# Optimization experiments

Measured on AMD Instinct MI355X. Metric: run time of the kernel, lower is better.

## Reference

```python
import jax, jax.numpy as jnp
import numpy as np

B, Lq, Lkv = 4, 1024, 4096
Cq, Ckv, E, NH = 512, 512, 512, 8
HD = E // NH


def setup_inputs() -> dict:
    key = jax.random.key(0)
    ks = jax.random.split(key, 8)
    s = 0.02
    return {
        "Xq": jax.random.normal(ks[0], (B, Lq, Cq), dtype=jnp.float32),
        "Xkv": jax.random.normal(ks[1], (B, Lkv, Ckv), dtype=jnp.float32),
        "mask": jax.random.randint(ks[2], (B, Lq, 1), 0, 2, dtype=jnp.int32),
        "Wq": jax.random.normal(ks[3], (Cq, E), dtype=jnp.float32) * s,
        "bq": jnp.zeros((E,), dtype=jnp.float32),
        "Wkv": jax.random.normal(ks[4], (Ckv, 2 * E), dtype=jnp.float32) * s,
        "bkv": jnp.zeros((2 * E,), dtype=jnp.float32),
        "Wp": jax.random.normal(ks[5], (E, E), dtype=jnp.float32) * s,
        "bp": jnp.zeros((E,), dtype=jnp.float32),
        "attn_pos": jax.random.normal(ks[6], (1, NH, Lq, Lkv), dtype=jnp.float32) * s,
    }


def reference(Xq, Xkv, mask, Wq, bq, Wkv, bkv, Wp, bp, attn_pos):
    scale = HD ** -0.5
    # projections
    Q = (Xq @ Wq + bq).reshape(B, Lq, NH, HD).transpose(0, 2, 1, 3) * scale  # [B,NH,Lq,HD]
    KV = (Xkv @ Wkv + bkv).reshape(B, Lkv, 2, NH, HD)
    K = KV[:, :, 0].transpose(0, 2, 1, 3)  # [B,NH,Lkv,HD]
    V = KV[:, :, 1].transpose(0, 2, 1, 3)
    # scores + learned positional bias
    attn = jnp.einsum('bhqd,bhkd->bhqk', Q, K) + attn_pos  # [B,NH,Lq,Lkv]
    # dummy-column masked softmax (mask: [B,Lq,1], 1=keep row)
    m = mask.astype(attn.dtype)[:, None]           # [B,1,Lq,1]
    attn = attn + (1.0 - m) * (-100.0)             # suppress masked query rows
    dummy = jnp.broadcast_to(jnp.where(m == 0, 100.0, -100.0), (B, NH, Lq, 1))
    attn = jax.nn.softmax(jnp.concatenate([attn, dummy], axis=-1), axis=-1)[..., :Lkv]
    # weighted sum + output projection (dropout = identity in eval)
    out = jnp.einsum('bhqk,bhkd->bhqd', attn, V)
    out = out.transpose(0, 2, 1, 3).reshape(B, Lq, E)
    return out @ Wp + bp
```

## Files before the change

### kernel.cpp

```cpp
#include <hip/hip_runtime.h>

typedef unsigned short u16;
typedef __attribute__((ext_vector_type(8))) short bf16x8;
typedef __attribute__((ext_vector_type(4))) float f32x4;
typedef __attribute__((ext_vector_type(2))) unsigned u32x2;
typedef __attribute__((ext_vector_type(4))) unsigned u32x4;

__device__ __forceinline__ u16 f2bf(float x) {
    union { float f; unsigned u; } v; v.f = x;
    unsigned r = v.u + 0x7FFF + ((v.u >> 16) & 1);
    return (u16)(r >> 16);
}

__device__ __forceinline__ unsigned cvt_pk_bf16(float lo, float hi) {
    unsigned r;
    asm("v_cvt_pk_bf16_f32 %0, %1, %2" : "=v"(r) : "v"(lo), "v"(hi));
    return r;
}

__device__ __forceinline__ void gl_lds16(const u16* g, u16* l) {
    __builtin_amdgcn_global_load_lds((const __attribute__((address_space(1))) void*)g,
                                     (__attribute__((address_space(3))) void*)l, 16, 0, 0);
}

__global__ __launch_bounds__(256) void conv_bf16(const float* __restrict__ in,
                                                 u16* __restrict__ out) {
    size_t i = ((size_t)blockIdx.x * 256 + threadIdx.x) * 8;
    const float4* p = (const float4*)(in + i);
    float4 a = p[0], b = p[1];
    u32x4 w = {cvt_pk_bf16(a.x, a.y), cvt_pk_bf16(a.z, a.w),
               cvt_pk_bf16(b.x, b.y), cvt_pk_bf16(b.z, b.w)};
    *(u32x4*)(out + i) = w;
}

__global__ __launch_bounds__(256) void transpose_w(const float* __restrict__ in,
                                                   u16* __restrict__ out, int R, int C) {
    __shared__ float tile[64][65];
    int r0 = blockIdx.y * 64, c0 = blockIdx.x * 64;
    int tid = threadIdx.x;
#pragma unroll
    for (int j = 0; j < 16; ++j) {
        int e = tid + j * 256;
        int row = e >> 6, col = e & 63;
        tile[row][col] = in[(size_t)(r0 + row) * C + c0 + col];
    }
    __syncthreads();
#pragma unroll
    for (int j = 0; j < 16; ++j) {
        int e = tid + j * 256;
        int row = e >> 6, col = e & 63;
        out[(size_t)(c0 + row) * R + r0 + col] = f2bf(tile[col][row]);
    }
}

__global__ __launch_bounds__(256) void transpose_v(const u16* __restrict__ in,
                                                   u16* __restrict__ out) {
    __shared__ u16 tile[64][65];
    int bh = blockIdx.y;
    int r0 = blockIdx.x * 64;
    const u16* ip = in + (size_t)bh * 4096 * 64;
    u16* op = out + (size_t)bh * 64 * 4096;
    int tid = threadIdx.x;
#pragma unroll
    for (int j = 0; j < 16; ++j) {
        int e = tid + j * 256;
        int row = e >> 6, col = e & 63;
        tile[row][col] = ip[(size_t)(r0 + row) * 64 + col];
    }
    __syncthreads();
#pragma unroll
    for (int j = 0; j < 16; ++j) {
        int e = tid + j * 256;
        int row = e >> 6, col = e & 63;
        op[(size_t)row * 4096 + r0 + col] = tile[col][row];
    }
}

template <int MODE>
__global__ __launch_bounds__(256) void gemm_kernel(const u16* __restrict__ A,
                                                   const u16* __restrict__ Bt,
                                                   const float* __restrict__ bias,
                                                   void* __restrict__ Cout,
                                                   void* __restrict__ Cout2,
                                                   int M, int N, int K) {
    __shared__ u16 Al[128][64];
    __shared__ u16 Bl[128][64];
    int tid = threadIdx.x;
    int lane = tid & 63, wid = tid >> 6;
    int wr = wid >> 1, wc = wid & 1;
    int l15 = lane & 15, g = lane >> 4;
    int bm = blockIdx.y, bn = blockIdx.x;
    int ldr = lane >> 3, ldc = (lane & 7) << 3;

    f32x4 acc[4][4];
#pragma unroll
    for (int m = 0; m < 4; ++m)
#pragma unroll
        for (int n = 0; n < 4; ++n)
#pragma unroll
            for (int j = 0; j < 4; ++j) acc[m][n][j] = 0.f;

    int nK = K >> 6;
    for (int kt = 0; kt < nK; ++kt) {
        __syncthreads();
#pragma unroll
        for (int i = 0; i < 4; ++i) {
            int c = wid * 4 + i;
            int row = c * 8 + ldr;
            gl_lds16(A + (size_t)(bm * 128 + row) * K + kt * 64 + ldc, &Al[0][0] + c * 512);
            gl_lds16(Bt + (size_t)(bn * 128 + row) * K + kt * 64 + ldc, &Bl[0][0] + c * 512);
        }
        __syncthreads();

#pragma unroll
        for (int kk = 0; kk < 2; ++kk) {
            bf16x8 af[4], bfr[4];
#pragma unroll
            for (int m = 0; m < 4; ++m)
                af[m] = *(const bf16x8*)&Al[wr * 64 + m * 16 + l15][kk * 32 + g * 8];
#pragma unroll
            for (int n = 0; n < 4; ++n)
                bfr[n] = *(const bf16x8*)&Bl[wc * 64 + n * 16 + l15][kk * 32 + g * 8];
#pragma unroll
            for (int m = 0; m < 4; ++m)
#pragma unroll
                for (int n = 0; n < 4; ++n)
                    acc[m][n] =
                        __builtin_amdgcn_mfma_f32_16x16x32_bf16(af[m], bfr[n], acc[m][n], 0, 0, 0);
        }
    }

#pragma unroll
    for (int m = 0; m < 4; ++m)
#pragma unroll
        for (int n = 0; n < 4; ++n)
#pragma unroll
            for (int j = 0; j < 4; ++j) {
                int row = bm * 128 + wr * 64 + m * 16 + g * 4 + j;
                int col = bn * 128 + wc * 64 + n * 16 + l15;
                float v = acc[m][n][j] + bias[col];
                if (MODE == 0) {
                    int b = row >> 10, q = row & 1023, h = col >> 6, d = col & 63;
                    ((u16*)Cout)[(((size_t)((b * 8 + h) * 1024 + q)) << 6) + d] =
                        f2bf(v * 0.18033688011112042f);
                } else if (MODE == 1) {
                    int b = row >> 12, kv = row & 4095;
                    int d = col & 63;
                    if (col < 512) {
                        int h = col >> 6;
                        ((u16*)Cout)[(((size_t)((b * 8 + h) * 4096 + kv)) << 6) + d] = f2bf(v);
                    } else {
                        int h = (col - 512) >> 6;
                        ((u16*)Cout2)[(((size_t)((b * 8 + h) * 4096 + kv)) << 6) + d] = f2bf(v);
                    }
                } else {
                    ((float*)Cout)[(size_t)row * N + col] = v;
                }
            }
}

__global__ __launch_bounds__(256, 2) void attn_kernel(const u16* __restrict__ Qb,
                                                      const u16* __restrict__ Kb,
                                                      const u16* __restrict__ Vt,
                                                      const float* __restrict__ pos,
                                                      float* __restrict__ Opart,
                                                      float* __restrict__ Lp) {
    __shared__ u16 Klds[4][4096];
    __shared__ u16 Vlds[4][4096];
    __shared__ u16 Plds[4][16][72];

    int idx = blockIdx.x;
    int h = idx & 7;
    int rest = idx >> 3;
    int qt = rest & 15, sp = rest >> 4;
    int q0 = qt * 64;
    int kvbase = sp * 1024;
    int tid = threadIdx.x, lane = tid & 63, wid = tid >> 6;
    int l15 = lane & 15, g = lane >> 4;

    bf16x8 aq[4][2];
#pragma unroll
    for (int b = 0; b < 4; ++b) {
        const u16* qp =
            Qb + (((size_t)((b * 8 + h) * 1024 + q0 + wid * 16 + l15)) << 6) + g * 8;
        aq[b][0] = *(const bf16x8*)(qp);
        aq[b][1] = *(const bf16x8*)(qp + 32);
    }

    f32x4 o[4][4];
    f32x4 lacc[4];
#pragma unroll
    for (int b = 0; b < 4; ++b) {
#pragma unroll
        for (int j = 0; j < 4; ++j) lacc[b][j] = 0.f;
#pragma unroll
        for (int n = 0; n < 4; ++n)
#pragma unroll
            for (int j = 0; j < 4; ++j) o[b][n][j] = 0.f;
    }

    const u16* Kg = Kb + ((size_t)(wid * 8 + h)) * 4096 * 64;
    const u16* Vg = Vt + ((size_t)(wid * 8 + h)) * 4096 * 64;
    u16* KldsW = &Klds[wid][0];
    u16* VldsW = &Vlds[wid][0];
    int lr = lane >> 3;
    int lcs = ((lane & 7) ^ lr) << 3;

    const float* posq =
        pos + (size_t)h * 1024 * 4096 + (size_t)(q0 + wid * 16 + l15) * 4096 + kvbase;

    const short one_s = (short)0x3F80;
    bf16x8 ones = {one_s, one_s, one_s, one_s, one_s, one_s, one_s, one_s};
    int sw = (l15 & 7) << 4;

    f32x4 zr[4];
    for (int kt = 0; kt < 16; ++kt) {
        int kv0 = kvbase + kt * 64;
        __syncthreads();
#pragma unroll
        for (int c = 0; c < 8; ++c)
            gl_lds16(Kg + (size_t)(kv0 + c * 8 + lr) * 64 + lcs, KldsW + c * 512);
#pragma unroll
        for (int c = 0; c < 8; ++c)
            gl_lds16(Vg + (size_t)(c * 8 + lr) * 4096 + kv0 + lcs, VldsW + c * 512);
#pragma unroll
        for (int n = 0; n < 4; ++n) {
            zr[n] = *(const f32x4*)(posq + kt * 64 + n * 16 + g * 4);
#pragma unroll
            for (int j = 0; j < 4; ++j) zr[n][j] *= 1.44269504f;
        }
        __syncthreads();

#pragma unroll
        for (int b = 0; b < 4; ++b) {
            const char* KbL = (const char*)&Klds[b][0];
            const char* VbL = (const char*)&Vlds[b][0];

            f32x4 s[4];
            __builtin_amdgcn_s_setprio(1);
#pragma unroll
            for (int n = 0; n < 4; ++n) {
                bf16x8 kb0 = *(const bf16x8*)(KbL + (n * 16 + l15) * 128 + ((g * 16) ^ sw));
                bf16x8 kb1 = *(const bf16x8*)(KbL + (n * 16 + l15) * 128 + ((64 + g * 16) ^ sw));
                f32x4 t = __builtin_amdgcn_mfma_f32_16x16x32_bf16(kb0, aq[b][0], zr[n], 0, 0, 0);
                s[n] = __builtin_amdgcn_mfma_f32_16x16x32_bf16(kb1, aq[b][1], t, 0, 0, 0);
            }
            __builtin_amdgcn_s_setprio(0);

#pragma unroll
            for (int n = 0; n < 4; ++n)
#pragma unroll
                for (int j = 0; j < 4; ++j)
                    s[n][j] = __builtin_exp2f(fminf(s[n][j], 80.f));

#pragma unroll
            for (int n = 0; n < 4; ++n) {
                u32x2 w;
                w.x = cvt_pk_bf16(s[n][0], s[n][1]);
                w.y = cvt_pk_bf16(s[n][2], s[n][3]);
                *(u32x2*)&Plds[wid][l15][n * 16 + g * 4] = w;
            }
            asm volatile("" ::: "memory");
            bf16x8 pa0 = *(const bf16x8*)&Plds[wid][l15][g * 8];
            bf16x8 pa1 = *(const bf16x8*)&Plds[wid][l15][32 + g * 8];
            asm volatile("" ::: "memory");

            __builtin_amdgcn_s_setprio(1);
#pragma unroll
            for (int n = 0; n < 4; ++n) {
                bf16x8 vb0 = *(const bf16x8*)(VbL + (n * 16 + l15) * 128 + ((g * 16) ^ sw));
                bf16x8 vb1 = *(const bf16x8*)(VbL + (n * 16 + l15) * 128 + ((64 + g * 16) ^ sw));
                o[b][n] = __builtin_amdgcn_mfma_f32_16x16x32_bf16(pa0, vb0, o[b][n], 0, 0, 0);
                o[b][n] = __builtin_amdgcn_mfma_f32_16x16x32_bf16(pa1, vb1, o[b][n], 0, 0, 0);
            }
            lacc[b] = __builtin_amdgcn_mfma_f32_16x16x32_bf16(pa0, ones, lacc[b], 0, 0, 0);
            lacc[b] = __builtin_amdgcn_mfma_f32_16x16x32_bf16(pa1, ones, lacc[b], 0, 0, 0);
            __builtin_amdgcn_s_setprio(0);
        }
    }

#pragma unroll
    for (int b = 0; b < 4; ++b) {
        int obase = (sp * 32 + b * 8 + h) * 1024;
#pragma unroll
        for (int j = 0; j < 4; ++j) {
            int row = q0 + wid * 16 + g * 4 + j;
#pragma unroll
            for (int n = 0; n < 4; ++n)
                Opart[((size_t)(obase + row)) * 64 + n * 16 + l15] = o[b][n][j];
            if (l15 == 0) Lp[obase + row] = lacc[b][j];
        }
    }
}

__global__ __launch_bounds__(256) void attn_combine(const float* __restrict__ Opart,
                                                    const float* __restrict__ Lp,
                                                    const int* __restrict__ mask,
                                                    u16* __restrict__ AO) {
    int tid = threadIdx.x;
    int d = tid & 63;
    int r = blockIdx.x * 4 + (tid >> 6);
    int bh = r >> 10, q = r & 1023;
    int b = bh >> 3, h = bh & 7;

    float L = 0.f, val = 0.f;
#pragma unroll
    for (int s2 = 0; s2 < 4; ++s2) {
        size_t rr = (size_t)(s2 * 32 + bh) * 1024 + q;
        L += Lp[rr];
        val += Opart[rr * 64 + d];
    }
    float res = mask[b * 1024 + q] ? (val / L) : 0.f;
    AO[((size_t)(b * 1024 + q)) * 512 + h * 64 + d] = f2bf(res);
}

extern "C" void kernel_launch(void* const* d_in, const int* in_sizes, int n_in,
                              void* d_out, int out_size, void* d_ws, size_t ws_size,
                              hipStream_t stream) {
    const float* Xq = (const float*)d_in[0];
    const float* Xkv = (const float*)d_in[1];
    const int* mask = (const int*)d_in[2];
    const float* Wq = (const float*)d_in[3];
    const float* bq = (const float*)d_in[4];
    const float* Wkv = (const float*)d_in[5];
    const float* bkv = (const float*)d_in[6];
    const float* Wp = (const float*)d_in[7];
    const float* bp = (const float*)d_in[8];
    const float* pos = (const float*)d_in[9];
    float* out = (float*)d_out;

    char* ws = (char*)d_ws;
    u16* WqT = (u16*)(ws);
    u16* WkvT = (u16*)(ws + 524288);
    u16* WpT = (u16*)(ws + 1572864);
    u16* Qb = (u16*)(ws + 2097152);
    u16* Kb = (u16*)(ws + 6291456);
    u16* Vt = (u16*)(ws + 23068672);
    u16* AO = (u16*)(ws + 39845888);
    float* Opart = (float*)(ws + 44040192);
    u16* Xkvb = (u16*)(ws + 44040192);
    u16* Vtm = (u16*)(ws + 60817408);
    u16* Xqb = (u16*)(ws + 77594624);
    float* Lp = (float*)(ws + 111149056);

    conv_bf16<<<dim3(1024), 256, 0, stream>>>(Xq, Xqb);
    conv_bf16<<<dim3(4096), 256, 0, stream>>>(Xkv, Xkvb);
    transpose_w<<<dim3(8, 8), 256, 0, stream>>>(Wq, WqT, 512, 512);
    transpose_w<<<dim3(16, 8), 256, 0, stream>>>(Wkv, WkvT, 512, 1024);
    transpose_w<<<dim3(8, 8), 256, 0, stream>>>(Wp, WpT, 512, 512);
    gemm_kernel<0><<<dim3(4, 32), 256, 0, stream>>>(Xqb, WqT, bq, Qb, nullptr, 4096, 512, 512);
    gemm_kernel<1><<<dim3(8, 128), 256, 0, stream>>>(Xkvb, WkvT, bkv, Kb, Vtm, 16384, 1024, 512);
    transpose_v<<<dim3(64, 32), 256, 0, stream>>>(Vtm, Vt);
    attn_kernel<<<dim3(512), 256, 0, stream>>>(Qb, Kb, Vt, pos, Opart, Lp);
    attn_combine<<<dim3(8192), 256, 0, stream>>>(Opart, Lp, mask, AO);
    gemm_kernel<2><<<dim3(4, 32), 256, 0, stream>>>(AO, WpT, bp, out, nullptr, 4096, 512, 512);
}
```

Before: 191.9 us.

## Restructure attention kernel with double-buffered KV tiles and per-wave batch split

Rewrites the attention kernel to use 512-thread blocks with 32 query rows, where each wave handles one batch and one 16-row slice, over 32-wide KV tiles. K and V tiles are double-buffered so the next tile's global-to-LDS load overlaps the current tile's compute. The positional bias for the next tile is prefetched into registers. The P matrix stays in registers because the V transpose kernel now writes a permuted column order that matches the MFMA output layout, which removes the LDS round-trip. Partial outputs are written with nontemporal stores. The changes aim to hide memory latency and raise occupancy, at the cost of twice as many barriers and a dependence on the exact permutation matching the MFMA layout.

Measured after the change: 279.8 us. 45.8% more time.

```diff
diff --git a/kernel.cpp b/kernel.cpp
--- a/kernel.cpp
+++ b/kernel.cpp
@@ -16,6 +16,15 @@
     unsigned r;
     asm("v_cvt_pk_bf16_f32 %0, %1, %2" : "=v"(r) : "v"(lo), "v"(hi));
     return r;
+}
+
+__device__ __forceinline__ bf16x8 pk8(const f32x4& s0, const f32x4& s1) {
+    union { u32x4 u; bf16x8 v; } x;
+    x.u[0] = cvt_pk_bf16(s0[0], s0[1]);
+    x.u[1] = cvt_pk_bf16(s0[2], s0[3]);
+    x.u[2] = cvt_pk_bf16(s1[0], s1[1]);
+    x.u[3] = cvt_pk_bf16(s1[2], s1[3]);
+    return x.v;
 }
 
 __device__ __forceinline__ void gl_lds16(const u16* g, u16* l) {
@@ -72,7 +81,9 @@
     for (int j = 0; j < 16; ++j) {
         int e = tid + j * 256;
         int row = e >> 6, col = e & 63;
-        op[(size_t)row * 4096 + r0 + col] = tile[col][row];
+        int c5 = col & 31;
+        int src = (col & 32) | ((((c5 >> 2) & 1) << 4) + ((c5 >> 3) << 2) + (c5 & 3));
+        op[(size_t)row * 4096 + r0 + col] = tile[src][row];
     }
 }
 
@@ -159,137 +170,139 @@
             }
 }
 
-__global__ __launch_bounds__(256, 2) void attn_kernel(const u16* __restrict__ Qb,
+__global__ __launch_bounds__(512, 4) void attn_kernel(const u16* __restrict__ Qb,
                                                       const u16* __restrict__ Kb,
                                                       const u16* __restrict__ Vt,
                                                       const float* __restrict__ pos,
                                                       float* __restrict__ Opart,
                                                       float* __restrict__ Lp) {
-    __shared__ u16 Klds[4][4096];
-    __shared__ u16 Vlds[4][4096];
-    __shared__ u16 Plds[4][16][72];
+    __shared__ u16 Kl[2][4][2048];
+    __shared__ u16 Vl[2][4][2048];
 
     int idx = blockIdx.x;
     int h = idx & 7;
     int rest = idx >> 3;
-    int qt = rest & 15, sp = rest >> 4;
-    int q0 = qt * 64;
-    int kvbase = sp * 1024;
+    int qt = rest & 31, sp = rest >> 5;
+    int q0 = qt * 32;
+    int kvb = sp * 1024;
     int tid = threadIdx.x, lane = tid & 63, wid = tid >> 6;
+    int b = wid & 3, mh = wid >> 2;
     int l15 = lane & 15, g = lane >> 4;
 
-    bf16x8 aq[4][2];
-#pragma unroll
-    for (int b = 0; b < 4; ++b) {
-        const u16* qp =
-            Qb + (((size_t)((b * 8 + h) * 1024 + q0 + wid * 16 + l15)) << 6) + g * 8;
-        aq[b][0] = *(const bf16x8*)(qp);
-        aq[b][1] = *(const bf16x8*)(qp + 32);
-    }
-
-    f32x4 o[4][4];
-    f32x4 lacc[4];
-#pragma unroll
-    for (int b = 0; b < 4; ++b) {
-#pragma unroll
-        for (int j = 0; j < 4; ++j) lacc[b][j] = 0.f;
-#pragma unroll
-        for (int n = 0; n < 4; ++n)
-#pragma unroll
-            for (int j = 0; j < 4; ++j) o[b][n][j] = 0.f;
-    }
-
-    const u16* Kg = Kb + ((size_t)(wid * 8 + h)) * 4096 * 64;
-    const u16* Vg = Vt + ((size_t)(wid * 8 + h)) * 4096 * 64;
-    u16* KldsW = &Klds[wid][0];
-    u16* VldsW = &Vlds[wid][0];
+    const size_t bh = (size_t)(b * 8 + h);
+    const u16* Kg = Kb + bh * (4096 * 64);
+    const u16* Vg = Vt + bh * (4096 * 64);
+    const u16* Qg = Qb + bh * (1024 * 64);
+
+    bf16x8 aq[2];
+    {
+        const u16* qp = Qg + (size_t)(q0 + mh * 16 + l15) * 64 + g * 8;
+        aq[0] = *(const bf16x8*)(qp);
+        aq[1] = *(const bf16x8*)(qp + 32);
+    }
+
+    f32x4 o[4], lacc;
+#pragma unroll
+    for (int j = 0; j < 4; ++j) lacc[j] = 0.f;
+#pragma unroll
+    for (int n = 0; n < 4; ++n)
+#pragma unroll
+        for (int j = 0; j < 4; ++j) o[n][j] = 0.f;
+
     int lr = lane >> 3;
-    int lcs = ((lane & 7) ^ lr) << 3;
-
-    const float* posq =
-        pos + (size_t)h * 1024 * 4096 + (size_t)(q0 + wid * 16 + l15) * 4096 + kvbase;
+    int swc = ((lane & 7) ^ lr) << 3;
+    int sx = l15 & 7;
+
+    auto STAGE = [&](int buf, int ktile) {
+        int kv0 = kvb + ktile * 32;
+        if (mh == 0) {
+#pragma unroll
+            for (int c = 0; c < 4; ++c)
+                gl_lds16(Kg + (size_t)(kv0 + c * 8 + lr) * 64 + swc, &Kl[buf][b][c * 512]);
+        } else {
+#pragma unroll
+            for (int c = 0; c < 4; ++c)
+                gl_lds16(Vg + (size_t)lane * 4096 + kv0 + c * 8, &Vl[buf][b][c * 512]);
+        }
+    };
+
+    const float* pp =
+        pos + (size_t)h * 4194304 + (size_t)(q0 + mh * 16 + l15) * 4096 + kvb + g * 4;
 
     const short one_s = (short)0x3F80;
     bf16x8 ones = {one_s, one_s, one_s, one_s, one_s, one_s, one_s, one_s};
-    int sw = (l15 & 7) << 4;
-
-    f32x4 zr[4];
-    for (int kt = 0; kt < 16; ++kt) {
-        int kv0 = kvbase + kt * 64;
+
+    STAGE(0, 0);
+    f32x4 zr[2];
+#pragma unroll
+    for (int n = 0; n < 2; ++n) {
+        zr[n] = *(const f32x4*)(pp + n * 16);
+#pragma unroll
+        for (int j = 0; j < 4; ++j) zr[n][j] *= 1.44269504f;
+    }
+
+    for (int kt = 0; kt < 32; ++kt) {
+        int cur = kt & 1;
         __syncthreads();
-#pragma unroll
-        for (int c = 0; c < 8; ++c)
-            gl_lds16(Kg + (size_t)(kv0 + c * 8 + lr) * 64 + lcs, KldsW + c * 512);
-#pragma unroll
-        for (int c = 0; c < 8; ++c)
-            gl_lds16(Vg + (size_t)(c * 8 + lr) * 4096 + kv0 + lcs, VldsW + c * 512);
-#pragma unroll
-        for (int n = 0; n < 4; ++n) {
-            zr[n] = *(const f32x4*)(posq + kt * 64 + n * 16 + g * 4);
-#pragma unroll
-            for (int j = 0; j < 4; ++j) zr[n][j] *= 1.44269504f;
-        }
-        __syncthreads();
-
-#pragma unroll
-        for (int b = 0; b < 4; ++b) {
-            const char* KbL = (const char*)&Klds[b][0];
-            const char* VbL = (const char*)&Vlds[b][0];
-
-            f32x4 s[4];
-            __builtin_amdgcn_s_setprio(1);
-#pragma unroll
-            for (int n = 0; n < 4; ++n) {
-                bf16x8 kb0 = *(const bf16x8*)(KbL + (n * 16 + l15) * 128 + ((g * 16) ^ sw));
-                bf16x8 kb1 = *(const bf16x8*)(KbL + (n * 16 + l15) * 128 + ((64 + g * 16) ^ sw));
-                f32x4 t = __builtin_amdgcn_mfma_f32_16x16x32_bf16(kb0, aq[b][0], zr[n], 0, 0, 0);
-                s[n] = __builtin_amdgcn_mfma_f32_16x16x32_bf16(kb1, aq[b][1], t, 0, 0, 0);
-            }
-            __builtin_amdgcn_s_setprio(0);
-
-#pragma unroll
-            for (int n = 0; n < 4; ++n)
-#pragma unroll
-                for (int j = 0; j < 4; ++j)
-                    s[n][j] = __builtin_exp2f(fminf(s[n][j], 80.f));
-
-#pragma unroll
-            for (int n = 0; n < 4; ++n) {
-                u32x2 w;
-                w.x = cvt_pk_bf16(s[n][0], s[n][1]);
-                w.y = cvt_pk_bf16(s[n][2], s[n][3]);
-                *(u32x2*)&Plds[wid][l15][n * 16 + g * 4] = w;
-            }
-            asm volatile("" ::: "memory");
-            bf16x8 pa0 = *(const bf16x8*)&Plds[wid][l15][g * 8];
-            bf16x8 pa1 = *(const bf16x8*)&Plds[wid][l15][32 + g * 8];
-            asm volatile("" ::: "memory");
-
-            __builtin_amdgcn_s_setprio(1);
-#pragma unroll
-            for (int n = 0; n < 4; ++n) {
-                bf16x8 vb0 = *(const bf16x8*)(VbL + (n * 16 + l15) * 128 + ((g * 16) ^ sw));
-                bf16x8 vb1 = *(const bf16x8*)(VbL + (n * 16 + l15) * 128 + ((64 + g * 16) ^ sw));
-                o[b][n] = __builtin_amdgcn_mfma_f32_16x16x32_bf16(pa0, vb0, o[b][n], 0, 0, 0);
-                o[b][n] = __builtin_amdgcn_mfma_f32_16x16x32_bf16(pa1, vb1, o[b][n], 0, 0, 0);
-            }
-            lacc[b] = __builtin_amdgcn_mfma_f32_16x16x32_bf16(pa0, ones, lacc[b], 0, 0, 0);
-            lacc[b] = __builtin_amdgcn_mfma_f32_16x16x32_bf16(pa1, ones, lacc[b], 0, 0, 0);
-            __builtin_amdgcn_s_setprio(0);
-        }
-    }
-
-#pragma unroll
-    for (int b = 0; b < 4; ++b) {
-        int obase = (sp * 32 + b * 8 + h) * 1024;
+        int kn = (kt + 1) & 31;
+        STAGE(cur ^ 1, kn);
+
+        const u16* Kc = &Kl[cur][b][0];
+        const u16* Vc = &Vl[cur][b][0];
+        bf16x8 kb[2][2], vb[4];
+#pragma unroll
+        for (int n = 0; n < 2; ++n) {
+            const u16* krow = Kc + (n * 16 + l15) * 64;
+            kb[n][0] = *(const bf16x8*)(krow + ((g ^ sx) << 3));
+            kb[n][1] = *(const bf16x8*)(krow + (((4 + g) ^ sx) << 3));
+        }
+#pragma unroll
+        for (int n = 0; n < 4; ++n)
+            vb[n] = *(const bf16x8*)(Vc + g * 512 + (n * 16 + l15) * 8);
+
+        f32x4 s[2];
+        __builtin_amdgcn_s_setprio(1);
+#pragma unroll
+        for (int n = 0; n < 2; ++n) {
+            f32x4 t = __builtin_amdgcn_mfma_f32_16x16x32_bf16(kb[n][0], aq[0], zr[n], 0, 0, 0);
+            s[n] = __builtin_amdgcn_mfma_f32_16x16x32_bf16(kb[n][1], aq[1], t, 0, 0, 0);
+        }
+        __builtin_amdgcn_s_setprio(0);
+
+        f32x4 z0 = *(const f32x4*)(pp + kn * 32);
+        f32x4 z1 = *(const f32x4*)(pp + kn * 32 + 16);
+
+#pragma unroll
+        for (int n = 0; n < 2; ++n)
+#pragma unroll
+            for (int j = 0; j < 4; ++j)
+                s[n][j] = __builtin_exp2f(fminf(s[n][j], 80.f));
+
+        bf16x8 pa = pk8(s[0], s[1]);
+
+        __builtin_amdgcn_s_setprio(1);
+#pragma unroll
+        for (int n = 0; n < 4; ++n)
+            o[n] = __builtin_amdgcn_mfma_f32_16x16x32_bf16(pa, vb[n], o[n], 0, 0, 0);
+        lacc = __builtin_amdgcn_mfma_f32_16x16x32_bf16(pa, ones, lacc, 0, 0, 0);
+        __builtin_amdgcn_s_setprio(0);
+
 #pragma unroll
         for (int j = 0; j < 4; ++j) {
-            int row = q0 + wid * 16 + g * 4 + j;
-#pragma unroll
-            for (int n = 0; n < 4; ++n)
-                Opart[((size_t)(obase + row)) * 64 + n * 16 + l15] = o[b][n][j];
-            if (l15 == 0) Lp[obase + row] = lacc[b][j];
-        }
+            zr[0][j] = z0[j] * 1.44269504f;
+            zr[1][j] = z1[j] * 1.44269504f;
+        }
+    }
+
+    int obase = (sp * 32 + b * 8 + h) * 1024;
+#pragma unroll
+    for (int j = 0; j < 4; ++j) {
+        int row = q0 + mh * 16 + g * 4 + j;
+#pragma unroll
+        for (int n = 0; n < 4; ++n)
+            __builtin_nontemporal_store(o[n][j],
+                                        &Opart[((size_t)(obase + row)) * 64 + n * 16 + l15]);
+        if (l15 == 0) __builtin_nontemporal_store(lacc[j], &Lp[obase + row]);
     }
 }
 
@@ -351,7 +364,7 @@
     gemm_kernel<0><<<dim3(4, 32), 256, 0, stream>>>(Xqb, WqT, bq, Qb, nullptr, 4096, 512, 512);
     gemm_kernel<1><<<dim3(8, 128), 256, 0, stream>>>(Xkvb, WkvT, bkv, Kb, Vtm, 16384, 1024, 512);
     transpose_v<<<dim3(64, 32), 256, 0, stream>>>(Vtm, Vt);
-    attn_kernel<<<dim3(512), 256, 0, stream>>>(Qb, Kb, Vt, pos, Opart, Lp);
+    attn_kernel<<<dim3(1024), 512, 0, stream>>>(Qb, Kb, Vt, pos, Opart, Lp);
     attn_combine<<<dim3(8192), 256, 0, stream>>>(Opart, Lp, mask, AO);
     gemm_kernel<2><<<dim3(4, 32), 256, 0, stream>>>(AO, WpT, bp, out, nullptr, 4096, 512, 512);
 }
```
